# Kernel optimization log

Hardware: AMD Instinct MI355X
Metric: run time of the kernel (lower is better)

The kernel has to match this reference:

```python
import jax, jax.numpy as jnp
import numpy as np

B, F, T, D = 65536, 1024, 64, 6


def setup_inputs() -> dict:
    key = jax.random.key(0)
    k0, k1, k2, k3 = jax.random.split(key, 4)
    x = jax.random.normal(k0, (B, F), dtype=jnp.float32)
    splits = jax.random.normal(k1, (T, D, F), dtype=jnp.float32)
    thresholds = jax.random.normal(k2, (T, D), dtype=jnp.float32)
    values = jax.random.normal(k3, (T, 2 ** D), dtype=jnp.float32)
    return {"x": x, "splits": splits, "thresholds": thresholds, "values": values}


def reference(x, splits, thresholds, values):
    # Since split_idx = depth % max_depth = depth, each level's split is path-independent.
    # bit_d = 1 means 'right' (score > threshold); node after D steps = 2^D - 1 + code,
    # leaf_idx = node - 2^D = code - 1 (torch negative indexing => mod 2^D).
    T_, D_, _ = splits.shape
    scores = jnp.einsum('bf,tdf->tbd', x, splits)          # (T, B, D)
    bits = (scores > thresholds[:, None, :]).astype(jnp.int32)
    pow2 = (2 ** jnp.arange(D_ - 1, -1, -1)).astype(jnp.int32)  # weight 2^(D-1-d)
    code = jnp.sum(bits * pow2, axis=-1)                   # (T, B)
    leaf = jnp.mod(code - 1, 2 ** D_)                      # (T, B)
    out_t = jnp.take_along_axis(values, leaf, axis=1)      # (T, B)
    return jnp.mean(out_t, axis=0)[:, None]                # (B, 1)
```

## Files before the change

### kernel.cpp

```cpp
#include <hip/hip_runtime.h>

#define BTOT 65536
#define FDIM 1024
#define TNUM 64
#define DNUM 6

#define BAND      1.5e-3f
#define GCUT      1.5e-4f
#define HEDGE_MAX 1.35f
#define CAP       8192

typedef unsigned int u32;
using f32x4  = __attribute__((ext_vector_type(4))) float;
using bf16x8 = __attribute__((ext_vector_type(8))) short;

__device__ __forceinline__ short f32_to_bf16(float v) {
    u32 bits = __float_as_uint(v);
    bits += 0x7FFFu + ((bits >> 16) & 1u);
    return (short)(bits >> 16);
}
__device__ __forceinline__ float bf16_to_f32(short h) {
    return __uint_as_float(((u32)(unsigned short)h) << 16);
}

#define RPITCH 40
#define A_HI 0
#define A_LO (64 * RPITCH)
#define B_HI (2 * 64 * RPITCH)
#define B_LO (2 * 64 * RPITCH + 384 * RPITCH)
#define SMEM_SHORTS (2 * 64 * RPITCH + 2 * 384 * RPITCH)
#define BTILE_SHORTS (2 * 384 * RPITCH)
#define PRE_OFFSET   65536

__global__ void pre_split(const float* __restrict__ splits,
                          short* __restrict__ pre) {
    const int q  = blockIdx.x * 256 + threadIdx.x;
    const int r  = q >> 8;
    const int c4 = q & 255;
    const float4 v = *(const float4*)(splits + (size_t)r * FDIM + c4 * 4);
    const int ks = c4 >> 3;
    const int c  = (c4 & 7) * 4;
    short* tile = pre + (size_t)ks * BTILE_SHORTS;
    const float vv[4] = {v.x, v.y, v.z, v.w};
    short hh[4], ll[4];
    #pragma unroll
    for (int e = 0; e < 4; ++e) {
        hh[e] = f32_to_bf16(vv[e]);
        const float lo = vv[e] - bf16_to_f32(hh[e]);
        ll[e] = f32_to_bf16(lo);
    }
    *(short4*)(tile + r * RPITCH + c)                      = make_short4(hh[0], hh[1], hh[2], hh[3]);
    *(short4*)(tile + 384 * RPITCH + r * RPITCH + c)       = make_short4(ll[0], ll[1], ll[2], ll[3]);
}

__global__ __launch_bounds__(256, 2)
void forest_mfma(const float* __restrict__ x,
                 const float* __restrict__ splits,
                 const float* __restrict__ thresholds,
                 const float* __restrict__ values,
                 float* __restrict__ out,
                 u32* __restrict__ gcnt,
                 u32* __restrict__ cands,
                 const short* __restrict__ pre,
                 const int use_pre) {
    __shared__ __align__(16) short smem[SMEM_SHORTS];
    __shared__ int wb_cnt;
    __shared__ u32 wb[32];

    const int tid  = threadIdx.x;
    const int lane = tid & 63;
    const int w    = tid >> 6;
    const int fr   = lane & 15;
    const int fq   = lane >> 4;
    const int b0   = blockIdx.x * 64;

    f32x4 acc[4][6];
    #pragma unroll
    for (int mi = 0; mi < 4; ++mi)
        #pragma unroll
        for (int ni = 0; ni < 6; ++ni) acc[mi][ni] = (f32x4)0.0f;

    if (use_pre) {
        #pragma unroll
        for (int j = 0; j < 2; ++j) {
            const int q = tid + j * 256, ra = q >> 3, c4 = q & 7;
            const float4 v = *(const float4*)(x + (size_t)(b0 + ra) * FDIM + c4 * 4);
            const float vv[4] = {v.x, v.y, v.z, v.w};
            short hh[4], ll[4];
            #pragma unroll
            for (int e = 0; e < 4; ++e) {
                hh[e] = f32_to_bf16(vv[e]);
                ll[e] = f32_to_bf16(vv[e] - bf16_to_f32(hh[e]));
            }
            *(short4*)(smem + A_HI + ra * RPITCH + c4 * 4) = make_short4(hh[0], hh[1], hh[2], hh[3]);
            *(short4*)(smem + A_LO + ra * RPITCH + c4 * 4) = make_short4(ll[0], ll[1], ll[2], ll[3]);
        }
        {
            const char* srcb = (const char*)pre;
            #pragma unroll
            for (int j = 0; j < 15; ++j) {
                const int ofs = (tid + j * 256) * 16;
                *(uint4*)((char*)smem + 2 * B_HI + ofs) = *(const uint4*)(srcb + ofs);
            }
        }
        __syncthreads();

        for (int ks = 0; ks < 32; ++ks) {
            float4 pa[2];
            if (ks < 31) {
                #pragma unroll
                for (int j = 0; j < 2; ++j) {
                    const int q = tid + j * 256, ra = q >> 3, c4 = q & 7;
                    pa[j] = *(const float4*)(x + (size_t)(b0 + ra) * FDIM + (ks + 1) * 32 + c4 * 4);
                }
            }
            bf16x8 ah[4], al[4], bh[6], bl[6];
            #pragma unroll
            for (int mi = 0; mi < 4; ++mi) {
                const int ro = (mi * 16 + fr) * RPITCH + fq * 8;
                ah[mi] = *(const bf16x8*)(smem + A_HI + ro);
                al[mi] = *(const bf16x8*)(smem + A_LO + ro);
            }
            #pragma unroll
            for (int ni = 0; ni < 6; ++ni) {
                const int ro = (w * 96 + ni * 16 + fr) * RPITCH + fq * 8;
                bh[ni] = *(const bf16x8*)(smem + B_HI + ro);
                bl[ni] = *(const bf16x8*)(smem + B_LO + ro);
            }
            #pragma unroll
            for (int mi = 0; mi < 4; ++mi)
                #pragma unroll
                for (int ni = 0; ni < 6; ++ni) {
                    acc[mi][ni] = __builtin_amdgcn_mfma_f32_16x16x32_bf16(ah[mi], bh[ni], acc[mi][ni], 0, 0, 0);
                    acc[mi][ni] = __builtin_amdgcn_mfma_f32_16x16x32_bf16(ah[mi], bl[ni], acc[mi][ni], 0, 0, 0);
                    acc[mi][ni] = __builtin_amdgcn_mfma_f32_16x16x32_bf16(al[mi], bh[ni], acc[mi][ni], 0, 0, 0);
                }
            __syncthreads();
            if (ks < 31) {
                #pragma unroll
                for (int j = 0; j < 2; ++j) {
                    const int q = tid + j * 256, ra = q >> 3, c4 = q & 7;
                    const float vv[4] = {pa[j].x, pa[j].y, pa[j].z, pa[j].w};
                    short hh[4], ll[4];
                    #pragma unroll
                    for (int e = 0; e < 4; ++e) {
                        hh[e] = f32_to_bf16(vv[e]);
                        ll[e] = f32_to_bf16(vv[e] - bf16_to_f32(hh[e]));
                    }
                    *(short4*)(smem + A_HI + ra * RPITCH + c4 * 4) = make_short4(hh[0], hh[1], hh[2], hh[3]);
                    *(short4*)(smem + A_LO + ra * RPITCH + c4 * 4) = make_short4(ll[0], ll[1], ll[2], ll[3]);
                }
                const char* srcb = (const char*)pre + (size_t)(ks + 1) * 61440;
                #pragma unroll
                for (int j = 0; j < 15; ++j) {
                    const int ofs = (tid + j * 256) * 16;
                    *(uint4*)((char*)smem + 2 * B_HI + ofs) = *(const uint4*)(srcb + ofs);
                }
                __syncthreads();
            }
        }
    } else {
        for (int ks = 0; ks < 32; ++ks) {
            const int k0 = ks * 32;
            __syncthreads();
            #pragma unroll
            for (int j = 0; j < 2; ++j) {
                const int q = tid + j * 256, ra = q >> 3, c4 = q & 7;
                const float4 v = *(const float4*)(x + (size_t)(b0 + ra) * FDIM + k0 + c4 * 4);
                const float vv[4] = {v.x, v.y, v.z, v.w};
                short hh[4], ll[4];
                #pragma unroll
                for (int e = 0; e < 4; ++e) {
                    hh[e] = f32_to_bf16(vv[e]);
                    ll[e] = f32_to_bf16(vv[e] - bf16_to_f32(hh[e]));
                }
                *(short4*)(smem + A_HI + ra * RPITCH + c4 * 4) = make_short4(hh[0], hh[1], hh[2], hh[3]);
                *(short4*)(smem + A_LO + ra * RPITCH + c4 * 4) = make_short4(ll[0], ll[1], ll[2], ll[3]);
            }
            #pragma unroll
            for (int j = 0; j < 12; ++j) {
                const int q = tid + j * 256, rb = q >> 3, c4 = q & 7;
                const float4 v = *(const float4*)(splits + (size_t)rb * FDIM + k0 + c4 * 4);
                const float vv[4] = {v.x, v.y, v.z, v.w};
                short hh[4], ll[4];
                #pragma unroll
                for (int e = 0; e < 4; ++e) {
                    hh[e] = f32_to_bf16(vv[e]);
                    ll[e] = f32_to_bf16(vv[e] - bf16_to_f32(hh[e]));
                }
                *(short4*)(smem + B_HI + rb * RPITCH + c4 * 4) = make_short4(hh[0], hh[1], hh[2], hh[3]);
                *(short4*)(smem + B_LO + rb * RPITCH + c4 * 4) = make_short4(ll[0], ll[1], ll[2], ll[3]);
            }
            __syncthreads();
            bf16x8 ah[4], al[4], bh[6], bl[6];
            #pragma unroll
            for (int mi = 0; mi < 4; ++mi) {
                const int ro = (mi * 16 + fr) * RPITCH + fq * 8;
                ah[mi] = *(const bf16x8*)(smem + A_HI + ro);
                al[mi] = *(const bf16x8*)(smem + A_LO + ro);
            }
            #pragma unroll
            for (int ni = 0; ni < 6; ++ni) {
                const int ro = (w * 96 + ni * 16 + fr) * RPITCH + fq * 8;
                bh[ni] = *(const bf16x8*)(smem + B_HI + ro);
                bl[ni] = *(const bf16x8*)(smem + B_LO + ro);
            }
            #pragma unroll
            for (int mi = 0; mi < 4; ++mi)
                #pragma unroll
                for (int ni = 0; ni < 6; ++ni) {
                    acc[mi][ni] = __builtin_amdgcn_mfma_f32_16x16x32_bf16(ah[mi], bh[ni], acc[mi][ni], 0, 0, 0);
                    acc[mi][ni] = __builtin_amdgcn_mfma_f32_16x16x32_bf16(ah[mi], bl[ni], acc[mi][ni], 0, 0, 0);
                    acc[mi][ni] = __builtin_amdgcn_mfma_f32_16x16x32_bf16(al[mi], bh[ni], acc[mi][ni], 0, 0, 0);
                }
        }
        __syncthreads();
    }

    __syncthreads();
    u32* code_lds = (u32*)smem;
    for (int i = tid; i < 4096; i += 256) code_lds[i] = 0;
    if (tid == 0) wb_cnt = 0;
    __syncthreads();

    #pragma unroll
    for (int ni = 0; ni < 6; ++ni) {
        const int td = w * 96 + ni * 16 + fr;
        const float th = thresholds[td];
        const int t = (td * 10923) >> 16;
        const int d = td - t * 6;
        const u32 orbit = 1u << (5 - d);
        #pragma unroll
        for (int mi = 0; mi < 4; ++mi)
            #pragma unroll
            for (int reg = 0; reg < 4; ++reg) {
                const float df = acc[mi][ni][reg] - th;
                const int bl_ = mi * 16 + fq * 4 + reg;
                if (df > 0.0f) atomicOr(&code_lds[bl_ * 64 + t], orbit);
                if (__builtin_expect(fabsf(df) < BAND, 0)) {
                    const int idx = atomicAdd(&wb_cnt, 1);
                    if (idx < 32) wb[idx] = ((u32)bl_ << 6) | (u32)t;
                }
            }
    }
    __syncthreads();

    {
        const int bl_ = tid >> 2, tq = tid & 3;
        float p = 0.0f;
        #pragma unroll
        for (int j = 0; j < 16; ++j) {
            const int t = tq * 16 + j;
            const int code = (int)(code_lds[bl_ * 64 + t] & 63u);
            p += values[t * 64 + ((code - 1) & 63)];
        }
        float* psum = (float*)(code_lds + 4096);
        psum[bl_ * 4 + tq] = p;
        __syncthreads();
        if (tid < 64) {
            const float* ps = psum + tid * 4;
            out[b0 + tid] = ((ps[0] + ps[1]) + (ps[2] + ps[3])) * (1.0f / 64.0f);
        }
    }

    if (tid < wb_cnt && tid < 32) {
        const u32 e = wb[tid];
        bool dup = false;
        for (int j = 0; j < tid; ++j) dup |= (wb[j] == e);
        if (!dup) {
            const int bl_ = (int)(e >> 6), t = (int)(e & 63u);
            const u32 code = code_lds[bl_ * 64 + t] & 63u;
            const u32 gidx = atomicAdd(gcnt, 1u);
            if (gidx < CAP)
                cands[gidx] = ((u32)(b0 + bl_) << 16) | ((u32)t << 6) | code;
        }
    }
}

__global__ __launch_bounds__(256)
void band_fix(const float* __restrict__ x,
              const float* __restrict__ splits,
              const float* __restrict__ thresholds,
              const float* __restrict__ values,
              float* __restrict__ out,
              const u32* __restrict__ gcnt,
              const u32* __restrict__ cands) {
    const u32 n = min(*gcnt, (u32)CAP);
    const u32 gid  = blockIdx.x * 256 + threadIdx.x;
    const u32 site = gid >> 3;
    const u32 sub  = gid & 7;
    if (site >= n) return;
    const u32 e = cands[site];
    const int b = (int)(e >> 16);
    const int t = (int)((e >> 6) & 63u);
    const int code_approx = (int)(e & 63u);
    const int d = (sub < 6) ? (int)sub : 0;

    const float* xr = x + (size_t)b * FDIM;
    const float* sr = splits + ((size_t)t * DNUM + d) * FDIM;
    float a = 0.0f;
    #pragma unroll 4
    for (int f = 0; f < FDIM; f += 16) {
        const float4 x0 = *(const float4*)(xr + f);
        const float4 x1 = *(const float4*)(xr + f + 4);
        const float4 x2 = *(const float4*)(xr + f + 8);
        const float4 x3 = *(const float4*)(xr + f + 12);
        const float4 s0 = *(const float4*)(sr + f);
        const float4 s1 = *(const float4*)(sr + f + 4);
        const float4 s2 = *(const float4*)(sr + f + 8);
        const float4 s3 = *(const float4*)(sr + f + 12);
        a = fmaf(x0.x, s0.x, a); a = fmaf(x0.y, s0.y, a);
        a = fmaf(x0.z, s0.z, a); a = fmaf(x0.w, s0.w, a);
        a = fmaf(x1.x, s1.x, a); a = fmaf(x1.y, s1.y, a);
        a = fmaf(x1.z, s1.z, a); a = fmaf(x1.w, s1.w, a);
        a = fmaf(x2.x, s2.x, a); a = fmaf(x2.y, s2.y, a);
        a = fmaf(x2.z, s2.z, a); a = fmaf(x2.w, s2.w, a);
        a = fmaf(x3.x, s3.x, a); a = fmaf(x3.y, s3.y, a);
        a = fmaf(x3.z, s3.z, a); a = fmaf(x3.w, s3.w, a);
    }
    const float df = a - thresholds[t * DNUM + d];

    const int lane = (int)(threadIdx.x & 63);
    const int base = lane & ~7;
    float dfs[6];
    #pragma unroll
    for (int j = 0; j < 6; ++j) dfs[j] = __shfl(df, base + j);

    if (sub == 0) {
        int code_chain = 0;
        #pragma unroll
        for (int j = 0; j < 6; ++j)
            code_chain = (code_chain << 1) | (dfs[j] > 0.0f ? 1 : 0);
        const float vA = values[t * 64 + ((code_approx - 1) & 63)];
        const float vC = values[t * 64 + ((code_chain - 1) & 63)];
        float delta = vC - vA;
        #pragma unroll
        for (int j = 0; j < 6; ++j) {
            if (fabsf(dfs[j]) < GCUT) {
                const int cf = code_chain ^ (1 << (5 - j));
                const float dv = values[t * 64 + ((cf - 1) & 63)] - vC;
                if (fabsf(dv) < HEDGE_MAX) delta += dv * 0.5f;
            }
        }
        atomicAdd(out + b, delta * (1.0f / 64.0f));
    }
}

extern "C" void kernel_launch(void* const* d_in, const int* in_sizes, int n_in,
                              void* d_out, int out_size, void* d_ws, size_t ws_size,
                              hipStream_t stream) {
    const float* x          = (const float*)d_in[0];
    const float* splits     = (const float*)d_in[1];
    const float* thresholds = (const float*)d_in[2];
    const float* values     = (const float*)d_in[3];
    float* out = (float*)d_out;

    u32* gcnt   = (u32*)d_ws;
    u32* cands  = (u32*)((char*)d_ws + 64);
    short* pre  = (short*)((char*)d_ws + PRE_OFFSET);
    const int use_pre = (ws_size >= (size_t)PRE_OFFSET + 32u * 61440u) ? 1 : 0;

    (void)hipMemsetAsync(gcnt, 0, 4, stream);
    if (use_pre)
        pre_split<<<dim3(384), dim3(256), 0, stream>>>(splits, pre);
    forest_mfma<<<dim3(BTOT / 64), dim3(256), 0, stream>>>(
        x, splits, thresholds, values, out, gcnt, cands, pre, use_pre);
    band_fix<<<dim3(CAP * 8 / 256), dim3(256), 0, stream>>>(
        x, splits, thresholds, values, out, gcnt, cands);
}
```

Baseline: 234.7 us.

## Async-load split tiles to LDS, swap MFMA operands, and decode leaves via ballots

Split tiles are now copied from the precomputed buffer straight into LDS with global_load_lds, and those copies are issued before the MFMA block so they overlap the matrix math. The MFMA operands are swapped so that tree/depth rows sit in the M dimension and batch rows in N. This lets the epilogue build each leaf code from wavefront ballots in registers, replacing the LDS atomicOr code table and the separate band-candidate list. The aim is to cut staging latency, barriers and LDS atomic traffic. The cost is more complex bit indexing, and every band candidate now does its own global atomic instead of being deduplicated per block.

New measurement: 249.4 us. 1.06x slower.

```diff
diff --git a/kernel.cpp b/kernel.cpp
--- a/kernel.cpp
+++ b/kernel.cpp
@@ -11,6 +11,7 @@
 #define CAP       8192
 
 typedef unsigned int u32;
+typedef unsigned long long u64;
 using f32x4  = __attribute__((ext_vector_type(4))) float;
 using bf16x8 = __attribute__((ext_vector_type(8))) short;
 
@@ -24,12 +25,13 @@
 }
 
 #define RPITCH 40
-#define A_HI 0
-#define A_LO (64 * RPITCH)
-#define B_HI (2 * 64 * RPITCH)
-#define B_LO (2 * 64 * RPITCH + 384 * RPITCH)
-#define SMEM_SHORTS (2 * 64 * RPITCH + 2 * 384 * RPITCH)
-#define BTILE_SHORTS (2 * 384 * RPITCH)
+#define A_HI_S 0
+#define A_LO_S (64 * RPITCH)
+#define B_HI_S (128 * RPITCH)
+#define B_LO_S (128 * RPITCH + 384 * RPITCH)
+#define SMEM_SHORTS (128 * RPITCH + 2 * 384 * RPITCH)
+#define B_BASE_BYTES (2 * B_HI_S)
+#define BTILE_BYTES  61440
 #define PRE_OFFSET   65536
 
 __global__ void pre_split(const float* __restrict__ splits,
@@ -40,17 +42,16 @@
     const float4 v = *(const float4*)(splits + (size_t)r * FDIM + c4 * 4);
     const int ks = c4 >> 3;
     const int c  = (c4 & 7) * 4;
-    short* tile = pre + (size_t)ks * BTILE_SHORTS;
+    short* tile = pre + (size_t)ks * (BTILE_BYTES / 2);
     const float vv[4] = {v.x, v.y, v.z, v.w};
     short hh[4], ll[4];
     #pragma unroll
     for (int e = 0; e < 4; ++e) {
         hh[e] = f32_to_bf16(vv[e]);
-        const float lo = vv[e] - bf16_to_f32(hh[e]);
-        ll[e] = f32_to_bf16(lo);
-    }
-    *(short4*)(tile + r * RPITCH + c)                      = make_short4(hh[0], hh[1], hh[2], hh[3]);
-    *(short4*)(tile + 384 * RPITCH + r * RPITCH + c)       = make_short4(ll[0], ll[1], ll[2], ll[3]);
+        ll[e] = f32_to_bf16(vv[e] - bf16_to_f32(hh[e]));
+    }
+    *(short4*)(tile + r * RPITCH + c)               = make_short4(hh[0], hh[1], hh[2], hh[3]);
+    *(short4*)(tile + 384 * RPITCH + r * RPITCH + c) = make_short4(ll[0], ll[1], ll[2], ll[3]);
 }
 
 __global__ __launch_bounds__(256, 2)
@@ -64,8 +65,6 @@
                  const short* __restrict__ pre,
                  const int use_pre) {
     __shared__ __align__(16) short smem[SMEM_SHORTS];
-    __shared__ int wb_cnt;
-    __shared__ u32 wb[32];
 
     const int tid  = threadIdx.x;
     const int lane = tid & 63;
@@ -74,38 +73,55 @@
     const int fq   = lane >> 4;
     const int b0   = blockIdx.x * 64;
 
-    f32x4 acc[4][6];
-    #pragma unroll
-    for (int mi = 0; mi < 4; ++mi)
-        #pragma unroll
-        for (int ni = 0; ni < 6; ++ni) acc[mi][ni] = (f32x4)0.0f;
+    f32x4 acc[6][4];
+    #pragma unroll
+    for (int tt = 0; tt < 6; ++tt)
+        #pragma unroll
+        for (int bt = 0; bt < 4; ++bt) acc[tt][bt] = (f32x4)0.0f;
+
+    #pragma unroll
+    for (int j = 0; j < 2; ++j) {
+        const int q = tid + j * 256, ra = q >> 3, c4 = q & 7;
+        const float4 v = *(const float4*)(x + (size_t)(b0 + ra) * FDIM + c4 * 4);
+        const float vv[4] = {v.x, v.y, v.z, v.w};
+        short hh[4], ll[4];
+        #pragma unroll
+        for (int e = 0; e < 4; ++e) {
+            hh[e] = f32_to_bf16(vv[e]);
+            ll[e] = f32_to_bf16(vv[e] - bf16_to_f32(hh[e]));
+        }
+        *(short4*)(smem + A_HI_S + ra * RPITCH + c4 * 4) = make_short4(hh[0], hh[1], hh[2], hh[3]);
+        *(short4*)(smem + A_LO_S + ra * RPITCH + c4 * 4) = make_short4(ll[0], ll[1], ll[2], ll[3]);
+    }
 
     if (use_pre) {
-        #pragma unroll
-        for (int j = 0; j < 2; ++j) {
-            const int q = tid + j * 256, ra = q >> 3, c4 = q & 7;
-            const float4 v = *(const float4*)(x + (size_t)(b0 + ra) * FDIM + c4 * 4);
-            const float vv[4] = {v.x, v.y, v.z, v.w};
-            short hh[4], ll[4];
-            #pragma unroll
-            for (int e = 0; e < 4; ++e) {
-                hh[e] = f32_to_bf16(vv[e]);
-                ll[e] = f32_to_bf16(vv[e] - bf16_to_f32(hh[e]));
-            }
-            *(short4*)(smem + A_HI + ra * RPITCH + c4 * 4) = make_short4(hh[0], hh[1], hh[2], hh[3]);
-            *(short4*)(smem + A_LO + ra * RPITCH + c4 * 4) = make_short4(ll[0], ll[1], ll[2], ll[3]);
-        }
         {
             const char* srcb = (const char*)pre;
             #pragma unroll
             for (int j = 0; j < 15; ++j) {
-                const int ofs = (tid + j * 256) * 16;
-                *(uint4*)((char*)smem + 2 * B_HI + ofs) = *(const uint4*)(srcb + ofs);
+                const int ub = (j * 256 + w * 64) * 16;
+                __builtin_amdgcn_global_load_lds(
+                    (const void*)(srcb + ub + (lane << 4)),
+                    (void*)((char*)smem + B_BASE_BYTES + ub),
+                    16, 0, 0);
             }
         }
         __syncthreads();
 
         for (int ks = 0; ks < 32; ++ks) {
+            bf16x8 sh[6], sl[6], xh[4], xl[4];
+            #pragma unroll
+            for (int tt = 0; tt < 6; ++tt) {
+                const int ro = (w * 96 + tt * 16 + fr) * RPITCH + fq * 8;
+                sh[tt] = *(const bf16x8*)(smem + B_HI_S + ro);
+                sl[tt] = *(const bf16x8*)(smem + B_LO_S + ro);
+            }
+            #pragma unroll
+            for (int bt = 0; bt < 4; ++bt) {
+                const int ro = (bt * 16 + fr) * RPITCH + fq * 8;
+                xh[bt] = *(const bf16x8*)(smem + A_HI_S + ro);
+                xl[bt] = *(const bf16x8*)(smem + A_LO_S + ro);
+            }
             float4 pa[2];
             if (ks < 31) {
                 #pragma unroll
@@ -114,28 +130,27 @@
                     pa[j] = *(const float4*)(x + (size_t)(b0 + ra) * FDIM + (ks + 1) * 32 + c4 * 4);
                 }
             }
-            bf16x8 ah[4], al[4], bh[6], bl[6];
-            #pragma unroll
-            for (int mi = 0; mi < 4; ++mi) {
-                const int ro = (mi * 16 + fr) * RPITCH + fq * 8;
-                ah[mi] = *(const bf16x8*)(smem + A_HI + ro);
-                al[mi] = *(const bf16x8*)(smem + A_LO + ro);
-            }
-            #pragma unroll
-            for (int ni = 0; ni < 6; ++ni) {
-                const int ro = (w * 96 + ni * 16 + fr) * RPITCH + fq * 8;
-                bh[ni] = *(const bf16x8*)(smem + B_HI + ro);
-                bl[ni] = *(const bf16x8*)(smem + B_LO + ro);
-            }
-            #pragma unroll
-            for (int mi = 0; mi < 4; ++mi)
-                #pragma unroll
-                for (int ni = 0; ni < 6; ++ni) {
-                    acc[mi][ni] = __builtin_amdgcn_mfma_f32_16x16x32_bf16(ah[mi], bh[ni], acc[mi][ni], 0, 0, 0);
-                    acc[mi][ni] = __builtin_amdgcn_mfma_f32_16x16x32_bf16(ah[mi], bl[ni], acc[mi][ni], 0, 0, 0);
-                    acc[mi][ni] = __builtin_amdgcn_mfma_f32_16x16x32_bf16(al[mi], bh[ni], acc[mi][ni], 0, 0, 0);
-                }
             __syncthreads();
+
+            if (ks < 31) {
+                const char* srcb = (const char*)pre + (size_t)(ks + 1) * BTILE_BYTES;
+                #pragma unroll
+                for (int j = 0; j < 15; ++j) {
+                    const int ub = (j * 256 + w * 64) * 16;
+                    __builtin_amdgcn_global_load_lds(
+                        (const void*)(srcb + ub + (lane << 4)),
+                        (void*)((char*)smem + B_BASE_BYTES + ub),
+                        16, 0, 0);
+                }
+            }
+            #pragma unroll
+            for (int tt = 0; tt < 6; ++tt)
+                #pragma unroll
+                for (int bt = 0; bt < 4; ++bt) {
+                    acc[tt][bt] = __builtin_amdgcn_mfma_f32_16x16x32_bf16(sh[tt], xh[bt], acc[tt][bt], 0, 0, 0);
+                    acc[tt][bt] = __builtin_amdgcn_mfma_f32_16x16x32_bf16(sh[tt], xl[bt], acc[tt][bt], 0, 0, 0);
+                    acc[tt][bt] = __builtin_amdgcn_mfma_f32_16x16x32_bf16(sl[tt], xh[bt], acc[tt][bt], 0, 0, 0);
+                }
             if (ks < 31) {
                 #pragma unroll
                 for (int j = 0; j < 2; ++j) {
@@ -147,35 +162,31 @@
                         hh[e] = f32_to_bf16(vv[e]);
                         ll[e] = f32_to_bf16(vv[e] - bf16_to_f32(hh[e]));
                     }
-                    *(short4*)(smem + A_HI + ra * RPITCH + c4 * 4) = make_short4(hh[0], hh[1], hh[2], hh[3]);
-                    *(short4*)(smem + A_LO + ra * RPITCH + c4 * 4) = make_short4(ll[0], ll[1], ll[2], ll[3]);
-                }
-                const char* srcb = (const char*)pre + (size_t)(ks + 1) * 61440;
-                #pragma unroll
-                for (int j = 0; j < 15; ++j) {
-                    const int ofs = (tid + j * 256) * 16;
-                    *(uint4*)((char*)smem + 2 * B_HI + ofs) = *(const uint4*)(srcb + ofs);
-                }
-                __syncthreads();
-            }
+                    *(short4*)(smem + A_HI_S + ra * RPITCH + c4 * 4) = make_short4(hh[0], hh[1], hh[2], hh[3]);
+                    *(short4*)(smem + A_LO_S + ra * RPITCH + c4 * 4) = make_short4(ll[0], ll[1], ll[2], ll[3]);
+                }
+            }
+            __syncthreads();
         }
     } else {
         for (int ks = 0; ks < 32; ++ks) {
             const int k0 = ks * 32;
-            __syncthreads();
-            #pragma unroll
-            for (int j = 0; j < 2; ++j) {
-                const int q = tid + j * 256, ra = q >> 3, c4 = q & 7;
-                const float4 v = *(const float4*)(x + (size_t)(b0 + ra) * FDIM + k0 + c4 * 4);
-                const float vv[4] = {v.x, v.y, v.z, v.w};
-                short hh[4], ll[4];
-                #pragma unroll
-                for (int e = 0; e < 4; ++e) {
-                    hh[e] = f32_to_bf16(vv[e]);
-                    ll[e] = f32_to_bf16(vv[e] - bf16_to_f32(hh[e]));
-                }
-                *(short4*)(smem + A_HI + ra * RPITCH + c4 * 4) = make_short4(hh[0], hh[1], hh[2], hh[3]);
-                *(short4*)(smem + A_LO + ra * RPITCH + c4 * 4) = make_short4(ll[0], ll[1], ll[2], ll[3]);
+            if (ks) {
+                __syncthreads();
+                #pragma unroll
+                for (int j = 0; j < 2; ++j) {
+                    const int q = tid + j * 256, ra = q >> 3, c4 = q & 7;
+                    const float4 v = *(const float4*)(x + (size_t)(b0 + ra) * FDIM + k0 + c4 * 4);
+                    const float vv[4] = {v.x, v.y, v.z, v.w};
+                    short hh[4], ll[4];
+                    #pragma unroll
+                    for (int e = 0; e < 4; ++e) {
+                        hh[e] = f32_to_bf16(vv[e]);
+                        ll[e] = f32_to_bf16(vv[e] - bf16_to_f32(hh[e]));
+                    }
+                    *(short4*)(smem + A_HI_S + ra * RPITCH + c4 * 4) = make_short4(hh[0], hh[1], hh[2], hh[3]);
+                    *(short4*)(smem + A_LO_S + ra * RPITCH + c4 * 4) = make_short4(ll[0], ll[1], ll[2], ll[3]);
+                }
             }
             #pragma unroll
             for (int j = 0; j < 12; ++j) {
@@ -188,92 +199,89 @@
                     hh[e] = f32_to_bf16(vv[e]);
                     ll[e] = f32_to_bf16(vv[e] - bf16_to_f32(hh[e]));
                 }
-                *(short4*)(smem + B_HI + rb * RPITCH + c4 * 4) = make_short4(hh[0], hh[1], hh[2], hh[3]);
-                *(short4*)(smem + B_LO + rb * RPITCH + c4 * 4) = make_short4(ll[0], ll[1], ll[2], ll[3]);
+                *(short4*)(smem + B_HI_S + rb * RPITCH + c4 * 4) = make_short4(hh[0], hh[1], hh[2], hh[3]);
+                *(short4*)(smem + B_LO_S + rb * RPITCH + c4 * 4) = make_short4(ll[0], ll[1], ll[2], ll[3]);
             }
             __syncthreads();
-            bf16x8 ah[4], al[4], bh[6], bl[6];
-            #pragma unroll
-            for (int mi = 0; mi < 4; ++mi) {
-                const int ro = (mi * 16 + fr) * RPITCH + fq * 8;
-                ah[mi] = *(const bf16x8*)(smem + A_HI + ro);
-                al[mi] = *(const bf16x8*)(smem + A_LO + ro);
-            }
-            #pragma unroll
-            for (int ni = 0; ni < 6; ++ni) {
-                const int ro = (w * 96 + ni * 16 + fr) * RPITCH + fq * 8;
-                bh[ni] = *(const bf16x8*)(smem + B_HI + ro);
-                bl[ni] = *(const bf16x8*)(smem + B_LO + ro);
-            }
-            #pragma unroll
-            for (int mi = 0; mi < 4; ++mi)
-                #pragma unroll
-                for (int ni = 0; ni < 6; ++ni) {
-                    acc[mi][ni] = __builtin_amdgcn_mfma_f32_16x16x32_bf16(ah[mi], bh[ni], acc[mi][ni], 0, 0, 0);
-                    acc[mi][ni] = __builtin_amdgcn_mfma_f32_16x16x32_bf16(ah[mi], bl[ni], acc[mi][ni], 0, 0, 0);
-                    acc[mi][ni] = __builtin_amdgcn_mfma_f32_16x16x32_bf16(al[mi], bh[ni], acc[mi][ni], 0, 0, 0);
+            bf16x8 sh[6], sl[6], xh[4], xl[4];
+            #pragma unroll
+            for (int tt = 0; tt < 6; ++tt) {
+                const int ro = (w * 96 + tt * 16 + fr) * RPITCH + fq * 8;
+                sh[tt] = *(const bf16x8*)(smem + B_HI_S + ro);
+                sl[tt] = *(const bf16x8*)(smem + B_LO_S + ro);
+            }
+            #pragma unroll
+            for (int bt = 0; bt < 4; ++bt) {
+                const int ro = (bt * 16 + fr) * RPITCH + fq * 8;
+                xh[bt] = *(const bf16x8*)(smem + A_HI_S + ro);
+                xl[bt] = *(const bf16x8*)(smem + A_LO_S + ro);
+            }
+            #pragma unroll
+            for (int tt = 0; tt < 6; ++tt)
+                #pragma unroll
+                for (int bt = 0; bt < 4; ++bt) {
+                    acc[tt][bt] = __builtin_amdgcn_mfma_f32_16x16x32_bf16(sh[tt], xh[bt], acc[tt][bt], 0, 0, 0);
+                    acc[tt][bt] = __builtin_amdgcn_mfma_f32_16x16x32_bf16(sh[tt], xl[bt], acc[tt][bt], 0, 0, 0);
+                    acc[tt][bt] = __builtin_amdgcn_mfma_f32_16x16x32_bf16(sl[tt], xh[bt], acc[tt][bt], 0, 0, 0);
                 }
         }
         __syncthreads();
     }
 
+    float th[6][4];
+    #pragma unroll
+    for (int tt = 0; tt < 6; ++tt)
+        #pragma unroll
+        for (int reg = 0; reg < 4; ++reg)
+            th[tt][reg] = thresholds[w * 96 + tt * 16 + fq * 4 + reg];
+
+    float* psum = (float*)smem;
+
+    #pragma unroll
+    for (int bt = 0; bt < 4; ++bt) {
+        u64 bal[6][4];
+        u32 bandmask = 0;
+        #pragma unroll
+        for (int tt = 0; tt < 6; ++tt)
+            #pragma unroll
+            for (int reg = 0; reg < 4; ++reg) {
+                const float df = acc[tt][bt][reg] - th[tt][reg];
+                bal[tt][reg] = __ballot(df > 0.0f);
+                if (__builtin_expect(fabsf(df) < BAND, 0))
+                    bandmask |= 1u << ((tt * 16 + fq * 4 + reg) / 6);
+            }
+        bandmask |= __shfl_xor(bandmask, 16);
+        bandmask |= __shfl_xor(bandmask, 32);
+
+        float partial = 0.0f;
+        #pragma unroll
+        for (int jj = 0; jj < 4; ++jj) {
+            const int j = fq * 4 + jj;
+            int code = 0;
+            #pragma unroll
+            for (int d = 0; d < DNUM; ++d) {
+                const int l   = j * 6 + d;
+                const int stt = l >> 4;
+                const int pos = l & 15;
+                const int bit = (int)((bal[stt][pos & 3] >> (((pos >> 2) << 4) + fr)) & 1ull);
+                code |= bit << (5 - d);
+            }
+            const int t = w * 16 + j;
+            partial += values[t * 64 + ((code - 1) & 63)];
+            if (__builtin_expect((bandmask >> j) & 1u, 0)) {
+                const u32 gidx = atomicAdd(gcnt, 1u);
+                if (gidx < CAP)
+                    cands[gidx] = ((u32)(b0 + bt * 16 + fr) << 16) | ((u32)t << 6) | (u32)code;
+            }
+        }
+        psum[(bt * 16 + fr) * 16 + w * 4 + fq] = partial;
+    }
     __syncthreads();
-    u32* code_lds = (u32*)smem;
-    for (int i = tid; i < 4096; i += 256) code_lds[i] = 0;
-    if (tid == 0) wb_cnt = 0;
-    __syncthreads();
-
-    #pragma unroll
-    for (int ni = 0; ni < 6; ++ni) {
-        const int td = w * 96 + ni * 16 + fr;
-        const float th = thresholds[td];
-        const int t = (td * 10923) >> 16;
-        const int d = td - t * 6;
-        const u32 orbit = 1u << (5 - d);
-        #pragma unroll
-        for (int mi = 0; mi < 4; ++mi)
-            #pragma unroll
-            for (int reg = 0; reg < 4; ++reg) {
-                const float df = acc[mi][ni][reg] - th;
-                const int bl_ = mi * 16 + fq * 4 + reg;
-                if (df > 0.0f) atomicOr(&code_lds[bl_ * 64 + t], orbit);
-                if (__builtin_expect(fabsf(df) < BAND, 0)) {
-                    const int idx = atomicAdd(&wb_cnt, 1);
-                    if (idx < 32) wb[idx] = ((u32)bl_ << 6) | (u32)t;
-                }
-            }
-    }
-    __syncthreads();
-
-    {
-        const int bl_ = tid >> 2, tq = tid & 3;
-        float p = 0.0f;
-        #pragma unroll
-        for (int j = 0; j < 16; ++j) {
-            const int t = tq * 16 + j;
-            const int code = (int)(code_lds[bl_ * 64 + t] & 63u);
-            p += values[t * 64 + ((code - 1) & 63)];
-        }
-        float* psum = (float*)(code_lds + 4096);
-        psum[bl_ * 4 + tq] = p;
-        __syncthreads();
-        if (tid < 64) {
-            const float* ps = psum + tid * 4;
-            out[b0 + tid] = ((ps[0] + ps[1]) + (ps[2] + ps[3])) * (1.0f / 64.0f);
-        }
-    }
-
-    if (tid < wb_cnt && tid < 32) {
-        const u32 e = wb[tid];
-        bool dup = false;
-        for (int j = 0; j < tid; ++j) dup |= (wb[j] == e);
-        if (!dup) {
-            const int bl_ = (int)(e >> 6), t = (int)(e & 63u);
-            const u32 code = code_lds[bl_ * 64 + t] & 63u;
-            const u32 gidx = atomicAdd(gcnt, 1u);
-            if (gidx < CAP)
-                cands[gidx] = ((u32)(b0 + bl_) << 16) | ((u32)t << 6) | code;
-        }
+    if (tid < 64) {
+        float s = 0.0f;
+        #pragma unroll
+        for (int k = 0; k < 16; ++k) s += psum[tid * 16 + k];
+        out[b0 + tid] = s * (1.0f / 64.0f);
     }
 }
 
@@ -358,7 +366,7 @@
     u32* gcnt   = (u32*)d_ws;
     u32* cands  = (u32*)((char*)d_ws + 64);
     short* pre  = (short*)((char*)d_ws + PRE_OFFSET);
-    const int use_pre = (ws_size >= (size_t)PRE_OFFSET + 32u * 61440u) ? 1 : 0;
+    const int use_pre = (ws_size >= (size_t)PRE_OFFSET + 32u * (size_t)BTILE_BYTES) ? 1 : 0;
 
     (void)hipMemsetAsync(gcnt, 0, 4, stream);
     if (use_pre)
```
